# Kernel tuning notes

Measured on AMD Instinct MI355X. Metric: run time of the kernel, lower is better.

Reference implementation:

```python
import jax, jax.numpy as jnp
import numpy as np

GRID_SIZE = 5
SPLINE_ORDER = 3
GRID_RANGE = (-1.0, 1.0)


def _make_grid():
    # knots: arange(-k, grid_size + k + 1) * h + lo -> 12 points for k=3, g=5
    h = (GRID_RANGE[1] - GRID_RANGE[0]) / GRID_SIZE
    return jnp.arange(-SPLINE_ORDER, GRID_SIZE + SPLINE_ORDER + 1, dtype=jnp.float32) * h + GRID_RANGE[0]


def _b_splines(x, grid):
    # x: (B, in) -> bases: (B, in, grid_size + spline_order) via Cox-de Boor
    x = x[..., None]  # (B, in, 1)
    bases = ((x >= grid[:-1]) & (x < grid[1:])).astype(x.dtype)
    for k in range(1, SPLINE_ORDER + 1):
        left = (x - grid[: -(k + 1)]) / (grid[k:-1] - grid[: -(k + 1)])
        right = (grid[k + 1:] - x) / (grid[k + 1:] - grid[1:-k])
        bases = left * bases[..., :-1] + right * bases[..., 1:]
    return bases


def _kan_linear(x, base_w, spline_w, spline_scaler, grid):
    # base path: SiLU(x) @ base_w.T
    base = jnp.einsum('bi,oi->bo', jax.nn.silu(x), base_w)
    # spline path: bases (B,in,K) contracted with scaled spline weight (out,in,K)
    bases = _b_splines(x, grid)
    scaled = spline_w * spline_scaler[..., None]
    spline = jnp.einsum('bik,oik->bo', bases, scaled)
    return base + spline


def setup_inputs() -> dict:
    key = jax.random.key(0)
    ks = jax.random.split(key, 9)
    B, D_in, H0, H1, L = 4096, 1024, 2048, 1024, 512
    K = GRID_SIZE + SPLINE_ORDER  # 8
    s = 0.05
    return {
        'x': jax.random.normal(ks[0], (B, D_in), jnp.float32),
        'bw0': jax.random.normal(ks[1], (H0, D_in), jnp.float32) * s,
        'sw0': jax.random.normal(ks[2], (H0, D_in, K), jnp.float32) * s,
        'ss0': jax.random.normal(ks[3], (H0, D_in), jnp.float32) * s,
        'bw1': jax.random.normal(ks[4], (H1, H0), jnp.float32) * s,
        'sw1': jax.random.normal(ks[5], (H1, H0, K), jnp.float32) * s,
        'ss1': jax.random.normal(ks[6], (H1, H0), jnp.float32) * s,
        'dw': jax.random.normal(ks[7], (L, H1), jnp.float32) * s,
        'db': jax.random.normal(ks[8], (L,), jnp.float32) * s,
    }


def reference(x, bw0, sw0, ss0, bw1, sw1, ss1, dw, db):
    grid = _make_grid()
    h = _kan_linear(x, bw0, sw0, ss0, grid)
    h = _kan_linear(h, bw1, sw1, ss1, grid)
    h = jax.nn.relu(h)
    return jnp.einsum('bi,oi->bo', h, dw) + db
```

## Files before the change

### kernel.cpp

```cpp
#include <hip/hip_runtime.h>
#include <cstdint>
#include <cstddef>


typedef __bf16 bf16x8 __attribute__((ext_vector_type(8)));
typedef float floatx4 __attribute__((ext_vector_type(4)));

#define BATCH 4096
#define DIN   1024
#define H0N   2048
#define H1N   1024
#define LOUT  512

#define OFF_A0  ((size_t)0)
#define OFF_W0  ((size_t)75497472)
#define OFF_A1  ((size_t)0)
#define OFF_P0  ((size_t)150994944)
#define OFF_W1  ((size_t)218103808)
#define OFF_P1  ((size_t)150994944)
#define OFF_H1R ((size_t)218103808)
#define OFF_DW  ((size_t)226492416)

__device__ __forceinline__ void bspline8(float x, float* out) {
    float b[11];
#pragma unroll
    for (int j = 0; j < 11; ++j) {
        float t0 = (j - 3) * 0.4f - 1.0f;
        float t1 = (j - 2) * 0.4f - 1.0f;
        b[j] = (x >= t0 && x < t1) ? 1.0f : 0.0f;
    }
#pragma unroll
    for (int k = 1; k <= 3; ++k) {
#pragma unroll
        for (int j = 0; j + k < 11; ++j) {
            float tj   = (j - 3) * 0.4f - 1.0f;
            float tj1  = (j - 2) * 0.4f - 1.0f;
            float tjk  = (j + k - 3) * 0.4f - 1.0f;
            float tjk1 = (j + k - 2) * 0.4f - 1.0f;
            float left  = (x - tj)   * (1.0f / (tjk - tj));
            float right = (tjk1 - x) * (1.0f / (tjk1 - tj1));
            b[j] = left * b[j] + right * b[j + 1];
        }
    }
#pragma unroll
    for (int j = 0; j < 8; ++j) out[j] = b[j];
}

__device__ __forceinline__ void coalesced_store9(__bf16* block_dst, const __bf16* vals) {
    __shared__ __bf16 sbuf[256 * 9];
    __bf16* p = &sbuf[threadIdx.x * 9];
#pragma unroll
    for (int j = 0; j < 9; ++j) p[j] = vals[j];
    __syncthreads();
    const uint4* src = (const uint4*)sbuf;
    uint4* dst = (uint4*)block_dst;
    dst[threadIdx.x] = src[threadIdx.x];
    if (threadIdx.x < 32) dst[256 + threadIdx.x] = src[256 + threadIdx.x];
}

__device__ __forceinline__ void act9(float v, __bf16* r) {
    float s = v / (1.0f + __expf(-v));
    float bb[8];
    bspline8(v, bb);
    r[0] = (__bf16)s;
#pragma unroll
    for (int j = 0; j < 8; ++j) r[1 + j] = (__bf16)bb[j];
}

__global__ void kan_act(const float* __restrict__ in, __bf16* __restrict__ out) {
    int base = blockIdx.x * 256;
    float v = in[base + threadIdx.x];
    __bf16 r[9];
    act9(v, r);
    coalesced_store9(out + (size_t)base * 9, r);
}

__global__ void kan_act_sum2(const float* __restrict__ pa, const float* __restrict__ pb,
                             __bf16* __restrict__ out) {
    int base = blockIdx.x * 256;
    int idx = base + threadIdx.x;
    float v = pa[idx] + pb[idx];
    __bf16 r[9];
    act9(v, r);
    coalesced_store9(out + (size_t)base * 9, r);
}

__global__ void relu_sum4(const float* __restrict__ p, size_t stride,
                          __bf16* __restrict__ out, int total4) {
    int idx = blockIdx.x * 256 + threadIdx.x;
    if (idx >= total4) return;
    const float4* p0 = (const float4*)p;
    const float4* p1 = (const float4*)(p + stride);
    const float4* p2 = (const float4*)(p + 2 * stride);
    const float4* p3 = (const float4*)(p + 3 * stride);
    float4 a = p0[idx], b = p1[idx], c = p2[idx], d = p3[idx];
    __bf16 r[4];
    r[0] = (__bf16)fmaxf(a.x + b.x + c.x + d.x, 0.0f);
    r[1] = (__bf16)fmaxf(a.y + b.y + c.y + d.y, 0.0f);
    r[2] = (__bf16)fmaxf(a.z + b.z + c.z + d.z, 0.0f);
    r[3] = (__bf16)fmaxf(a.w + b.w + c.w + d.w, 0.0f);
    *(uint2*)&out[(size_t)idx * 4] = *(uint2*)r;
}

__global__ void kan_wprep(const float* __restrict__ bw, const float* __restrict__ sw,
                          const float* __restrict__ ss, __bf16* __restrict__ out) {
    int base = blockIdx.x * 256;
    int idx = base + threadIdx.x;
    float b  = bw[idx];
    float sc = ss[idx];
    const float4* sv = (const float4*)(sw + (size_t)idx * 8);
    float4 a = sv[0], c = sv[1];
    __bf16 r[9];
    r[0] = (__bf16)b;
    r[1] = (__bf16)(a.x * sc); r[2] = (__bf16)(a.y * sc);
    r[3] = (__bf16)(a.z * sc); r[4] = (__bf16)(a.w * sc);
    r[5] = (__bf16)(c.x * sc); r[6] = (__bf16)(c.y * sc);
    r[7] = (__bf16)(c.z * sc); r[8] = (__bf16)(c.w * sc);
    coalesced_store9(out + (size_t)base * 9, r);
}

__global__ void f2bf(const float* __restrict__ in, __bf16* __restrict__ out,
                     int total) {
    int idx = blockIdx.x * 256 + threadIdx.x;
    if (idx < total) out[idx] = (__bf16)in[idx];
}

__device__ __forceinline__ void gload_lds16(const void* g, void* l) {
    __builtin_amdgcn_global_load_lds(
        (const __attribute__((address_space(1))) uint32_t*)g,
        (__attribute__((address_space(3))) uint32_t*)l, 16, 0, 0);
}

__global__ __launch_bounds__(256, 2) void gemm_big(
    const __bf16* __restrict__ A, const __bf16* __restrict__ W,
    float* __restrict__ Cout, int M, int N, int K, int Ks) {
    constexpr int BK = 32;
    __shared__ __bf16 As[2][256 * BK];
    __shared__ __bf16 Ws[2][128 * BK];

    const int tid  = threadIdx.x;
    const int lane = tid & 63;
    const int wave = tid >> 6;

    const int id    = (blockIdx.z * gridDim.y + blockIdx.y) * gridDim.x + blockIdx.x;
    const int mslab = gridDim.y >> 3;
    const int xcd   = id & 7;
    const int local = id >> 3;
    const int m_off = local % mslab;
    const int rest  = local / mslab;
    const int ntile = rest % gridDim.x;
    const int zt    = rest / gridDim.x;
    const int bm    = (xcd * mslab + m_off) * 256;
    const int bn    = ntile * 128;
    const int kbase = zt * Ks;

    const int wm = wave * 64;
    const int lr = lane & 15;
    const int ks = (lane >> 4) * 8;

    floatx4 acc[4][8] = {};

    auto stage = [&](int buf, int kpos) {
#pragma unroll
        for (int i = 0; i < 4; ++i) {
            int c = i * 256 + tid;
            int r = c >> 2;
            int s = (c & 3) * 8;
            gload_lds16(&A[(size_t)(bm + r) * K + kbase + kpos + s],
                        &As[buf][(size_t)(i * 256 + wave * 64) * 8]);
        }
#pragma unroll
        for (int i = 0; i < 2; ++i) {
            int c = i * 256 + tid;
            int r = c >> 2;
            int s = (c & 3) * 8;
            gload_lds16(&W[(size_t)(bn + r) * K + kbase + kpos + s],
                        &Ws[buf][(size_t)(i * 256 + wave * 64) * 8]);
        }
    };

    auto compute = [&](int buf) {
        bf16x8 af[4], wf[8];
#pragma unroll
        for (int t = 0; t < 4; ++t)
            af[t] = *(const bf16x8*)&As[buf][(wm + t * 16 + lr) * BK + ks];
#pragma unroll
        for (int t = 0; t < 8; ++t)
            wf[t] = *(const bf16x8*)&Ws[buf][(t * 16 + lr) * BK + ks];
#pragma unroll
        for (int mt = 0; mt < 4; ++mt)
#pragma unroll
            for (int nt = 0; nt < 8; ++nt)
                acc[mt][nt] = __builtin_amdgcn_mfma_f32_16x16x32_bf16(
                    af[mt], wf[nt], acc[mt][nt], 0, 0, 0);
    };

    stage(0, 0);
    for (int k0 = 0; k0 < Ks; k0 += 2 * BK) {
        __syncthreads();
        if (k0 + BK < Ks) stage(1, k0 + BK);
        compute(0);
        __syncthreads();
        if (k0 + 2 * BK < Ks) stage(0, k0 + 2 * BK);
        compute(1);
    }

    float* Cz = Cout + (size_t)zt * M * N;
    const int col = lane & 15;
    const int rquad = (lane >> 4) * 4;
#pragma unroll
    for (int mt = 0; mt < 4; ++mt) {
#pragma unroll
        for (int nt = 0; nt < 8; ++nt) {
            int n = bn + nt * 16 + col;
#pragma unroll
            for (int rg = 0; rg < 4; ++rg) {
                int m = bm + wm + mt * 16 + rquad + rg;
                Cz[(size_t)m * N + n] = acc[mt][nt][rg];
            }
        }
    }
}

__global__ __launch_bounds__(256) void gemm_dense(
    const __bf16* __restrict__ A, const __bf16* __restrict__ W,
    float* __restrict__ Cout, const float* __restrict__ bias,
    int M, int N, int K) {
    constexpr int BK = 32;
    __shared__ __bf16 As[2][128 * BK];
    __shared__ __bf16 Ws[2][128 * BK];

    const int tid  = threadIdx.x;
    const int lane = tid & 63;
    const int wave = tid >> 6;

    const int id    = blockIdx.y * gridDim.x + blockIdx.x;
    const int mslab = gridDim.y >> 3;
    const int xcd   = id & 7;
    const int local = id >> 3;
    const int m_off = local % mslab;
    const int ntile = local / mslab;
    const int bm    = (xcd * mslab + m_off) * 128;
    const int bn    = ntile * 128;

    const int wm = (wave >> 1) * 64;
    const int wn = (wave & 1) * 64;
    const int lr = lane & 15;
    const int ks = (lane >> 4) * 8;

    floatx4 acc[4][4] = {};

    auto stage = [&](int buf, int kpos) {
#pragma unroll
        for (int i = 0; i < 2; ++i) {
            int c = i * 256 + tid;
            int r = c >> 2;
            int s = (c & 3) * 8;
            gload_lds16(&A[(size_t)(bm + r) * K + kpos + s],
                        &As[buf][(size_t)(i * 256 + wave * 64) * 8]);
            gload_lds16(&W[(size_t)(bn + r) * K + kpos + s],
                        &Ws[buf][(size_t)(i * 256 + wave * 64) * 8]);
        }
    };

    auto compute = [&](int buf) {
        bf16x8 af[4], wf[4];
#pragma unroll
        for (int t = 0; t < 4; ++t) {
            af[t] = *(const bf16x8*)&As[buf][(wm + t * 16 + lr) * BK + ks];
            wf[t] = *(const bf16x8*)&Ws[buf][(wn + t * 16 + lr) * BK + ks];
        }
#pragma unroll
        for (int mt = 0; mt < 4; ++mt)
#pragma unroll
            for (int nt = 0; nt < 4; ++nt)
                acc[mt][nt] = __builtin_amdgcn_mfma_f32_16x16x32_bf16(
                    af[mt], wf[nt], acc[mt][nt], 0, 0, 0);
    };

    stage(0, 0);
    for (int k0 = 0; k0 < K; k0 += 2 * BK) {
        __syncthreads();
        if (k0 + BK < K) stage(1, k0 + BK);
        compute(0);
        __syncthreads();
        if (k0 + 2 * BK < K) stage(0, k0 + 2 * BK);
        compute(1);
    }

    const int col = lane & 15;
    const int rquad = (lane >> 4) * 4;
#pragma unroll
    for (int mt = 0; mt < 4; ++mt) {
#pragma unroll
        for (int nt = 0; nt < 4; ++nt) {
            int n = bn + wn + nt * 16 + col;
#pragma unroll
            for (int rg = 0; rg < 4; ++rg) {
                int m = bm + wm + mt * 16 + rquad + rg;
                Cout[(size_t)m * N + n] = acc[mt][nt][rg] + bias[n];
            }
        }
    }
}

extern "C" void kernel_launch(void* const* d_in, const int* in_sizes, int n_in,
                              void* d_out, int out_size, void* d_ws, size_t ws_size,
                              hipStream_t stream) {
    const float* x   = (const float*)d_in[0];
    const float* bw0 = (const float*)d_in[1];
    const float* sw0 = (const float*)d_in[2];
    const float* ss0 = (const float*)d_in[3];
    const float* bw1 = (const float*)d_in[4];
    const float* sw1 = (const float*)d_in[5];
    const float* ss1 = (const float*)d_in[6];
    const float* dw  = (const float*)d_in[7];
    const float* db  = (const float*)d_in[8];
    float* out = (float*)d_out;

    char* ws = (char*)d_ws;
    __bf16* A0  = (__bf16*)(ws + OFF_A0);
    __bf16* W0  = (__bf16*)(ws + OFF_W0);
    __bf16* A1  = (__bf16*)(ws + OFF_A1);
    float*  P0  = (float*)(ws + OFF_P0);
    __bf16* W1  = (__bf16*)(ws + OFF_W1);
    float*  P1  = (float*)(ws + OFF_P1);
    __bf16* h1r = (__bf16*)(ws + OFF_H1R);
    __bf16* dwb = (__bf16*)(ws + OFF_DW);

    kan_wprep<<<(H0N * DIN) / 256, 256, 0, stream>>>(bw0, sw0, ss0, W0);
    kan_act<<<(BATCH * DIN) / 256, 256, 0, stream>>>(x, A0);
    gemm_big<<<dim3(H0N / 128, BATCH / 256, 2), 256, 0, stream>>>(
        A0, W0, P0, BATCH, H0N, DIN * 9, DIN * 9 / 2);

    kan_wprep<<<(H1N * H0N) / 256, 256, 0, stream>>>(bw1, sw1, ss1, W1);
    kan_act_sum2<<<(BATCH * H0N) / 256, 256, 0, stream>>>(
        P0, P0 + (size_t)BATCH * H0N, A1);
    gemm_big<<<dim3(H1N / 128, BATCH / 256, 4), 256, 0, stream>>>(
        A1, W1, P1, BATCH, H1N, H0N * 9, H0N * 9 / 4);

    relu_sum4<<<(BATCH * H1N / 4) / 256, 256, 0, stream>>>(
        P1, (size_t)BATCH * H1N, h1r, BATCH * H1N / 4);

    f2bf<<<(LOUT * H1N) / 256, 256, 0, stream>>>(dw, dwb, LOUT * H1N);
    gemm_dense<<<dim3(LOUT / 128, BATCH / 128), 256, 0, stream>>>(
        h1r, dwb, out, db, BATCH, LOUT, H1N);
}
```

Measured before the change: 621.6 us.

## Load A fragments directly to registers and swizzle W tile in LDS

Drops the shared-memory staging of the A tile in the big GEMM. Each wave now loads its own A fragments straight from global memory into registers and double-buffers them across k-steps. The W tile stays in LDS but is XOR-swizzled to reduce bank conflicts on fragment reads. This cuts LDS traffic and LDS footprint. The cost is uncoalesced 16-byte global loads for A, more register pressure, and global latency exposed inside the loop. Note that aload(k0+BK) runs without the bounds guard that stageW has, which may read past the K slice.

```diff
diff --git a/kernel.cpp b/kernel.cpp
--- a/kernel.cpp
+++ b/kernel.cpp
@@ -135,7 +135,6 @@
     const __bf16* __restrict__ A, const __bf16* __restrict__ W,
     float* __restrict__ Cout, int M, int N, int K, int Ks) {
     constexpr int BK = 32;
-    __shared__ __bf16 As[2][256 * BK];
     __shared__ __bf16 Ws[2][128 * BK];
 
     const int tid  = threadIdx.x;
@@ -156,37 +155,38 @@
 
     const int wm = wave * 64;
     const int lr = lane & 15;
-    const int ks = (lane >> 4) * 8;
+    const int kq = lane >> 4;
+    const int ks = kq * 8;
 
     floatx4 acc[4][8] = {};
 
-    auto stage = [&](int buf, int kpos) {
-#pragma unroll
-        for (int i = 0; i < 4; ++i) {
-            int c = i * 256 + tid;
-            int r = c >> 2;
-            int s = (c & 3) * 8;
-            gload_lds16(&A[(size_t)(bm + r) * K + kbase + kpos + s],
-                        &As[buf][(size_t)(i * 256 + wave * 64) * 8]);
-        }
+    auto stageW = [&](int buf, int kpos) {
 #pragma unroll
         for (int i = 0; i < 2; ++i) {
             int c = i * 256 + tid;
             int r = c >> 2;
-            int s = (c & 3) * 8;
-            gload_lds16(&W[(size_t)(bn + r) * K + kbase + kpos + s],
+            int p = c & 3;
+            int q = p ^ ((r ^ (r >> 2)) & 3);
+            gload_lds16(&W[(size_t)(bn + r) * K + kbase + kpos + q * 8],
                         &Ws[buf][(size_t)(i * 256 + wave * 64) * 8]);
         }
     };
 
-    auto compute = [&](int buf) {
-        bf16x8 af[4], wf[8];
+    auto aload = [&](int kpos, bf16x8* af) {
 #pragma unroll
         for (int t = 0; t < 4; ++t)
-            af[t] = *(const bf16x8*)&As[buf][(wm + t * 16 + lr) * BK + ks];
-#pragma unroll
-        for (int t = 0; t < 8; ++t)
-            wf[t] = *(const bf16x8*)&Ws[buf][(t * 16 + lr) * BK + ks];
+            af[t] = *(const bf16x8*)&A[(size_t)(bm + wm + t * 16 + lr) * K +
+                                       kbase + kpos + ks];
+    };
+
+    auto compute = [&](int buf, const bf16x8* af) {
+        bf16x8 wf[8];
+#pragma unroll
+        for (int t = 0; t < 8; ++t) {
+            int r = t * 16 + lr;
+            int p = kq ^ ((r ^ (r >> 2)) & 3);
+            wf[t] = *(const bf16x8*)&Ws[buf][r * BK + p * 8];
+        }
 #pragma unroll
         for (int mt = 0; mt < 4; ++mt)
 #pragma unroll
@@ -195,14 +195,20 @@
                     af[mt], wf[nt], acc[mt][nt], 0, 0, 0);
     };
 
-    stage(0, 0);
+    bf16x8 afA[4], afB[4];
+    stageW(0, 0);
+    aload(0, afA);
     for (int k0 = 0; k0 < Ks; k0 += 2 * BK) {
         __syncthreads();
-        if (k0 + BK < Ks) stage(1, k0 + BK);
-        compute(0);
+        if (k0 + BK < Ks) stageW(1, k0 + BK);
+        aload(k0 + BK, afB);
+        compute(0, afA);
         __syncthreads();
-        if (k0 + 2 * BK < Ks) stage(0, k0 + 2 * BK);
-        compute(1);
+        if (k0 + 2 * BK < Ks) {
+            stageW(0, k0 + 2 * BK);
+            aload(k0 + 2 * BK, afA);
+        }
+        compute(1, afB);
     }
 
     float* Cz = Cout + (size_t)zt * M * N;
```

Result: slower. 654.9 us (+5.3%).
